# Performance work log

Measured on AMD Instinct MI355X. Metric: run time of the kernel, lower is better.

The kernel has to match this reference:

```python
import jax, jax.numpy as jnp
import numpy as np

B, S, HID = 4, 2048, 576
NH, NKV, HD = 9, 3, 64
MAXPOS, THETA = 8192, 100000.0


def rotate_half(x):
    x1, x2 = x[..., : x.shape[-1] // 2], x[..., x.shape[-1] // 2 :]
    return jnp.concatenate((-x2, x1), axis=-1)


def setup_inputs() -> dict:
    key = jax.random.key(0)
    ks = jax.random.split(key, 6)
    x = jax.random.normal(ks[0], (B, S, HID), dtype=jnp.float32)
    # RoPE tables (HuggingFace layout: freqs duplicated across halves)
    inv_freq = 1.0 / (THETA ** (np.arange(0, HD, 2, dtype=np.float32) / HD))
    freqs = np.outer(np.arange(MAXPOS, dtype=np.float32), inv_freq)
    emb = np.concatenate([freqs, freqs], axis=-1)
    cos = jnp.asarray(np.cos(emb))
    sin = jnp.asarray(np.sin(emb))
    position_ids = jnp.broadcast_to(jnp.arange(S, dtype=jnp.int64), (B, S))
    # additive causal mask [B,1,S,S]
    causal = jnp.where(
        jnp.tril(jnp.ones((S, S), dtype=bool)), 0.0, -1e9
    ).astype(jnp.float32)
    attention_mask = jnp.broadcast_to(causal, (B, 1, S, S))
    scale = 0.02
    wq = jax.random.normal(ks[1], (NH * HD, HID), dtype=jnp.float32) * scale
    wk = jax.random.normal(ks[2], (NKV * HD, HID), dtype=jnp.float32) * scale
    wv = jax.random.normal(ks[3], (NKV * HD, HID), dtype=jnp.float32) * scale
    wo = jax.random.normal(ks[4], (HID, NH * HD), dtype=jnp.float32) * scale
    return {
        "x": x, "cos": cos, "sin": sin, "position_ids": position_ids,
        "attention_mask": attention_mask,
        "wq": wq, "wk": wk, "wv": wv, "wo": wo,
    }


def reference(x, cos, sin, position_ids, attention_mask, wq, wk, wv, wo):
    b, s, _ = x.shape
    # projections (nn.Linear: y = x @ W.T), split into heads -> [B,H,S,D]
    q = (x @ wq.T).reshape(b, s, NH, HD).transpose(0, 2, 1, 3)
    k = (x @ wk.T).reshape(b, s, NKV, HD).transpose(0, 2, 1, 3)
    v = (x @ wv.T).reshape(b, s, NKV, HD).transpose(0, 2, 1, 3)
    # RoPE: cos/sin gathered per position -> [B,1,S,D], broadcast over heads
    c = cos[position_ids][:, None, :, :]
    si = sin[position_ids][:, None, :, :]
    q = q * c + rotate_half(q) * si
    k = k * c + rotate_half(k) * si
    # GQA expansion: repeat_interleave kv heads to match q heads
    k = jnp.repeat(k, NH // NKV, axis=1)
    v = jnp.repeat(v, NH // NKV, axis=1)
    scale = 1.0 / jnp.sqrt(jnp.asarray(HD, dtype=x.dtype))
    scores = jnp.einsum("bhqd,bhkd->bhqk", q, k) * scale + attention_mask
    attn = jax.nn.softmax(scores.astype(jnp.float32), axis=-1).astype(q.dtype)
    out = jnp.einsum("bhqk,bhkd->bhqd", attn, v)
    out = out.transpose(0, 2, 1, 3).reshape(b, s, NH * HD)
    return out @ wo.T
```

## Files before the change

### kernel.cpp

```cpp
#include <hip/hip_runtime.h>
#include <hip/hip_bf16.h>

#define B_    4
#define S_    2048
#define HID_  576
#define NH_   9
#define NKV_  3
#define HD_   64
#define GQ_   3

typedef __attribute__((ext_vector_type(8))) short bf16x8;
typedef __attribute__((ext_vector_type(4))) float f32x4;

__device__ __forceinline__ short f2bf(float f) {
    union { float f; unsigned int u; } v; v.f = f;
    unsigned int r = (v.u + 0x7fffu + ((v.u >> 16) & 1u)) >> 16;
    return (short)r;
}

__device__ __forceinline__ float exp2fast(float x) {
    return __builtin_amdgcn_exp2f(x);
}

__device__ __forceinline__ void async16(const void* g, void* l) {
    __builtin_amdgcn_global_load_lds(
        (const __attribute__((address_space(1))) unsigned int*)g,
        (__attribute__((address_space(3))) unsigned int*)l, 16, 0, 0);
}

#define NX_   (8192 * 576)
#define NWQ_  (576 * 576)
#define NWK_  (192 * 576)
#define NWV_  (192 * 576)
#define NWO_  (576 * 576)
#define NTOT_ (NX_ + NWQ_ + NWK_ + NWV_ + NWO_)

__global__ __launch_bounds__(256) void convert_kernel(
    const float* __restrict__ x,  const float* __restrict__ wq,
    const float* __restrict__ wk, const float* __restrict__ wv,
    const float* __restrict__ wo,
    short* __restrict__ xb, short* __restrict__ wqkvb, short* __restrict__ wob)
{
    int i4 = (blockIdx.x * 256 + threadIdx.x) * 4;
    const float* src; short* dst;
    if (i4 < NX_)                          { src = x  + i4;                          dst = xb    + i4; }
    else if (i4 < NX_ + NWQ_)              { src = wq + (i4 - NX_);                  dst = wqkvb + (i4 - NX_); }
    else if (i4 < NX_ + NWQ_ + NWK_)       { src = wk + (i4 - NX_ - NWQ_);           dst = wqkvb + (i4 - NX_); }
    else if (i4 < NX_ + NWQ_ + NWK_ + NWV_){ src = wv + (i4 - NX_ - NWQ_ - NWK_);    dst = wqkvb + (i4 - NX_); }
    else                                   { src = wo + (i4 - NX_ - NWQ_ - NWK_ - NWV_);
                                             dst = wob + (i4 - NX_ - NWQ_ - NWK_ - NWV_); }
    float4 v = *(const float4*)src;
    short4 o = make_short4(f2bf(v.x), f2bf(v.y), f2bf(v.z), f2bf(v.w));
    *(short4*)dst = o;
}

__global__ __launch_bounds__(256) void qkv_kernel(
    const short* __restrict__ xb,
    const short* __restrict__ wqkvb,
    const float* __restrict__ cosb,
    const float* __restrict__ sinb,
    short* __restrict__ Q,
    short* __restrict__ K,
    short* __restrict__ Vt)
{
    __shared__ __align__(16) short As[2][256 * 64];
    __shared__ __align__(16) short Bs[2][64 * 64];

    const int m0     = blockIdx.x * 256;
    const int nb_blk = blockIdx.y;
    const int tid  = threadIdx.x;
    const int w    = tid >> 6, lane = tid & 63;
    const int quad = lane >> 4, c = lane & 15;
    const int lr   = lane >> 3, lg = lane & 7;
    const int sw   = lg ^ lr;
    const int xg   = quad ^ (c & 7);

    auto stage = [&](int step, short* dstA, short* dstB) {
        const int k0 = step * 64;
        #pragma unroll
        for (int r = 0; r < 8; ++r) {
            int ch = w * 8 + r, R = ch * 8 + lr;
            async16(xb + (size_t)(m0 + R) * HID_ + k0 + sw * 8, (char*)dstA + ch * 1024);
        }
        #pragma unroll
        for (int r = 0; r < 2; ++r) {
            int ch = w * 2 + r, R = ch * 8 + lr;
            async16(wqkvb + (size_t)(nb_blk * 64 + R) * HID_ + k0 + sw * 8, (char*)dstB + ch * 1024);
        }
    };

    f32x4 acc[4][4];
    #pragma unroll
    for (int mt = 0; mt < 4; ++mt)
        #pragma unroll
        for (int nb = 0; nb < 4; ++nb) acc[mt][nb] = (f32x4){0.f, 0.f, 0.f, 0.f};

    stage(0, As[0], Bs[0]);

    int buf = 0;
    for (int kk = 0; kk < 9; ++kk) {
        __syncthreads();
        if (kk < 8) stage(kk + 1, As[buf ^ 1], Bs[buf ^ 1]);

        const short* a_s = As[buf];
        const short* b_s = Bs[buf];
        bf16x8 bfr[4][2];
        #pragma unroll
        for (int nb = 0; nb < 4; ++nb) {
            int row = nb * 16 + c;
            bfr[nb][0] = *(const bf16x8*)(b_s + row * 64 + xg * 8);
            bfr[nb][1] = *(const bf16x8*)(b_s + row * 64 + (xg ^ 4) * 8);
        }
        #pragma unroll
        for (int mt = 0; mt < 4; ++mt) {
            int row = w * 64 + mt * 16 + c;
            bf16x8 a0 = *(const bf16x8*)(a_s + row * 64 + xg * 8);
            bf16x8 a1 = *(const bf16x8*)(a_s + row * 64 + (xg ^ 4) * 8);
            #pragma unroll
            for (int nb = 0; nb < 4; ++nb) {
                acc[mt][nb] = __builtin_amdgcn_mfma_f32_16x16x32_bf16(a0, bfr[nb][0], acc[mt][nb], 0, 0, 0);
                acc[mt][nb] = __builtin_amdgcn_mfma_f32_16x16x32_bf16(a1, bfr[nb][1], acc[mt][nb], 0, 0, 0);
            }
        }
        buf ^= 1;
    }

    int type, head;
    if (nb_blk < NH_)            { type = 0; head = nb_blk; }
    else if (nb_blk < NH_ + NKV_){ type = 1; head = nb_blk - NH_; }
    else                         { type = 2; head = nb_blk - NH_ - NKV_; }
    const int b  = m0 >> 11;
    const int s0 = m0 & (S_ - 1);

    if (type < 2) {
        const float qs = (type == 0) ? 0.18033688f : 1.0f;
        #pragma unroll
        for (int mt = 0; mt < 4; ++mt)
            #pragma unroll
            for (int reg = 0; reg < 4; ++reg) {
                int s = s0 + w * 64 + mt * 16 + quad * 4 + reg;
                const float* cr = cosb + (size_t)s * HD_;
                const float* sr = sinb + (size_t)s * HD_;
                float a0 = acc[mt][0][reg], a1 = acc[mt][1][reg];
                float a2 = acc[mt][2][reg], a3 = acc[mt][3][reg];
                float o0 = (a0 * cr[c]      - a2 * sr[c])      * qs;
                float o1 = (a1 * cr[c + 16] - a3 * sr[c + 16]) * qs;
                float o2 = (a2 * cr[c + 32] + a0 * sr[c + 32]) * qs;
                float o3 = (a3 * cr[c + 48] + a1 * sr[c + 48]) * qs;
                short* dst = (type == 0)
                    ? Q + (((size_t)b * NH_  + head) * S_ + s) * HD_
                    : K + (((size_t)b * NKV_ + head) * S_ + s) * HD_;
                dst[c]      = f2bf(o0);
                dst[c + 16] = f2bf(o1);
                dst[c + 32] = f2bf(o2);
                dst[c + 48] = f2bf(o3);
            }
    } else {
        short* base = Vt + (((size_t)b * NKV_ + head) * HD_) * S_;
        #pragma unroll
        for (int mt = 0; mt < 4; ++mt) {
            int s4 = s0 + w * 64 + mt * 16 + quad * 4;
            #pragma unroll
            for (int nb = 0; nb < 4; ++nb) {
                int d = nb * 16 + c;
                short4 pk = make_short4(f2bf(acc[mt][nb][0]), f2bf(acc[mt][nb][1]),
                                        f2bf(acc[mt][nb][2]), f2bf(acc[mt][nb][3]));
                *(short4*)(base + (size_t)d * S_ + s4) = pk;
            }
        }
    }
}

#define PSTR 72

__global__ __launch_bounds__(256) void attn_kernel(
    const short* __restrict__ Q,
    const short* __restrict__ K,
    const short* __restrict__ Vt,
    short* __restrict__ AOb)
{
    __shared__ __align__(16) short Qs[64 * 64];
    __shared__ __align__(16) short Ks[2][64 * 64];
    __shared__ __align__(16) short Vs[2][64 * 64];
    __shared__ __align__(16) short Ps[64 * PSTR];

    const int hb = blockIdx.x;
    const int h  = hb >> 2, b = hb & 3;
    const int qt = 31 - blockIdx.y;
    const int kh = h / GQ_;
    const int tid  = threadIdx.x;
    const int w    = tid >> 6, lane = tid & 63;
    const int quad = lane >> 4, c = lane & 15;
    const int lr   = lane >> 3, lg = lane & 7;
    const int sw   = lg ^ lr;
    const int xg   = quad ^ (c & 7);

    const short* Qg = Q  + (((size_t)b * NH_  + h ) * S_ + qt * 64) * HD_;
    const short* Kg = K  + (((size_t)b * NKV_ + kh) * S_) * HD_;
    const short* Vg = Vt + (((size_t)b * NKV_ + kh) * HD_) * S_;

    #pragma unroll
    for (int r = 0; r < 2; ++r) {
        int ch = w * 2 + r, R = ch * 8 + lr;
        async16(Qg + (size_t)R * HD_ + sw * 8, (char*)Qs + ch * 1024);
    }
    #pragma unroll
    for (int r = 0; r < 4; ++r) {
        int it = w * 4 + r;
        if (it < 8) {
            int R = it * 8 + lr;
            async16(Kg + (size_t)R * HD_ + sw * 8, (char*)Ks[0] + it * 1024);
        } else {
            int R = (it - 8) * 8 + lr;
            async16(Vg + (size_t)R * S_ + sw * 8, (char*)Vs[0] + (it - 8) * 1024);
        }
    }

    bf16x8 ones;
    #pragma unroll
    for (int i = 0; i < 8; ++i) ones[i] = (short)0x3F80;

    f32x4 acc_o[4];
    #pragma unroll
    for (int nb = 0; nb < 4; ++nb) acc_o[nb] = (f32x4){0.f, 0.f, 0.f, 0.f};
    f32x4 acc_l = (f32x4){0.f, 0.f, 0.f, 0.f};

    bf16x8 aq0, aq1;

    auto do_tile = [&](const short* ks, const short* vs, bool MASK) {
        f32x4 sc[4];
        #pragma unroll
        for (int nb = 0; nb < 4; ++nb) {
            bf16x8 bk0 = *(const bf16x8*)(ks + (nb * 16 + c) * 64 + xg * 8);
            bf16x8 bk1 = *(const bf16x8*)(ks + (nb * 16 + c) * 64 + (xg ^ 4) * 8);
            f32x4 z = (f32x4){0.f, 0.f, 0.f, 0.f};
            z = __builtin_amdgcn_mfma_f32_16x16x32_bf16(aq0, bk0, z, 0, 0, 0);
            z = __builtin_amdgcn_mfma_f32_16x16x32_bf16(aq1, bk1, z, 0, 0, 0);
            sc[nb] = z;
        }
        #pragma unroll
        for (int r = 0; r < 4; ++r) {
            const int qrow = w * 16 + quad * 4 + r;
            #pragma unroll
            for (int nb = 0; nb < 4; ++nb) {
                float sv = sc[nb][r] - 4.0f;
                if (MASK && (nb * 16 + c > qrow)) sv = -1e30f;
                Ps[(w * 16 + quad * 4 + r) * PSTR + nb * 16 + c] = f2bf(exp2fast(sv));
            }
        }
        #pragma unroll
        for (int kc = 0; kc < 2; ++kc) {
            bf16x8 ap = *(const bf16x8*)(Ps + (w * 16 + c) * PSTR + quad * 8 + kc * 32);
            int pg = kc ? (xg ^ 4) : xg;
            #pragma unroll
            for (int nb = 0; nb < 4; ++nb) {
                bf16x8 bv = *(const bf16x8*)(vs + (nb * 16 + c) * 64 + pg * 8);
                acc_o[nb] = __builtin_amdgcn_mfma_f32_16x16x32_bf16(ap, bv, acc_o[nb], 0, 0, 0);
            }
            acc_l = __builtin_amdgcn_mfma_f32_16x16x32_bf16(ap, ones, acc_l, 0, 0, 0);
        }
    };

    __syncthreads();
    aq0 = *(const bf16x8*)(Qs + (w * 16 + c) * 64 + xg * 8);
    aq1 = *(const bf16x8*)(Qs + (w * 16 + c) * 64 + (xg ^ 4) * 8);

    int buf = 0;
    for (int kt = 0; kt < qt; ++kt) {
        int nxt = buf ^ 1;
        #pragma unroll
        for (int r = 0; r < 4; ++r) {
            int it = w * 4 + r;
            if (it < 8) {
                int R = it * 8 + lr;
                async16(Kg + (size_t)((kt + 1) * 64 + R) * HD_ + sw * 8,
                        (char*)Ks[nxt] + it * 1024);
            } else {
                int R = (it - 8) * 8 + lr;
                async16(Vg + (size_t)R * S_ + (kt + 1) * 64 + sw * 8,
                        (char*)Vs[nxt] + (it - 8) * 1024);
            }
        }
        do_tile(Ks[buf], Vs[buf], false);
        __syncthreads();
        buf ^= 1;
    }
    do_tile(Ks[buf], Vs[buf], true);

    #pragma unroll
    for (int r = 0; r < 4; ++r) {
        int s = qt * 64 + w * 16 + quad * 4 + r;
        float inv = 1.f / acc_l[r];
        short* dst = AOb + (((size_t)b * S_ + s) * NH_ + h) * HD_;
        #pragma unroll
        for (int nb = 0; nb < 4; ++nb)
            dst[nb * 16 + c] = f2bf(acc_o[nb][r] * inv);
    }
}

__global__ __launch_bounds__(256) void oproj_kernel(
    const short* __restrict__ AOb,
    const short* __restrict__ wob,
    float* __restrict__ out)
{
    __shared__ __align__(16) short As[2][256 * 64];
    __shared__ __align__(16) short Bs[2][64 * 64];

    const int m0 = blockIdx.x * 256;
    const int n0 = blockIdx.y * 64;
    const int tid  = threadIdx.x;
    const int w    = tid >> 6, lane = tid & 63;
    const int quad = lane >> 4, c = lane & 15;
    const int lr   = lane >> 3, lg = lane & 7;
    const int sw   = lg ^ lr;
    const int xg   = quad ^ (c & 7);

    auto stage = [&](int step, short* dstA, short* dstB) {
        const int k0 = step * 64;
        #pragma unroll
        for (int r = 0; r < 8; ++r) {
            int ch = w * 8 + r, R = ch * 8 + lr;
            async16(AOb + (size_t)(m0 + R) * HID_ + k0 + sw * 8, (char*)dstA + ch * 1024);
        }
        #pragma unroll
        for (int r = 0; r < 2; ++r) {
            int ch = w * 2 + r, R = ch * 8 + lr;
            async16(wob + (size_t)(n0 + R) * HID_ + k0 + sw * 8, (char*)dstB + ch * 1024);
        }
    };

    f32x4 acc[4][4];
    #pragma unroll
    for (int mt = 0; mt < 4; ++mt)
        #pragma unroll
        for (int nb = 0; nb < 4; ++nb) acc[mt][nb] = (f32x4){0.f, 0.f, 0.f, 0.f};

    stage(0, As[0], Bs[0]);

    int buf = 0;
    for (int kk = 0; kk < 9; ++kk) {
        __syncthreads();
        if (kk < 8) stage(kk + 1, As[buf ^ 1], Bs[buf ^ 1]);

        const short* a_s = As[buf];
        const short* b_s = Bs[buf];
        bf16x8 bfr[4][2];
        #pragma unroll
        for (int nb = 0; nb < 4; ++nb) {
            int row = nb * 16 + c;
            bfr[nb][0] = *(const bf16x8*)(b_s + row * 64 + xg * 8);
            bfr[nb][1] = *(const bf16x8*)(b_s + row * 64 + (xg ^ 4) * 8);
        }
        #pragma unroll
        for (int mt = 0; mt < 4; ++mt) {
            int row = w * 64 + mt * 16 + c;
            bf16x8 a0 = *(const bf16x8*)(a_s + row * 64 + xg * 8);
            bf16x8 a1 = *(const bf16x8*)(a_s + row * 64 + (xg ^ 4) * 8);
            #pragma unroll
            for (int nb = 0; nb < 4; ++nb) {
                acc[mt][nb] = __builtin_amdgcn_mfma_f32_16x16x32_bf16(a0, bfr[nb][0], acc[mt][nb], 0, 0, 0);
                acc[mt][nb] = __builtin_amdgcn_mfma_f32_16x16x32_bf16(a1, bfr[nb][1], acc[mt][nb], 0, 0, 0);
            }
        }
        buf ^= 1;
    }

    #pragma unroll
    for (int mt = 0; mt < 4; ++mt)
        #pragma unroll
        for (int reg = 0; reg < 4; ++reg) {
            int m = m0 + w * 64 + mt * 16 + quad * 4 + reg;
            float* dst = out + (size_t)m * HID_ + n0;
            #pragma unroll
            for (int nb = 0; nb < 4; ++nb)
                dst[nb * 16 + c] = acc[mt][nb][reg];
        }
}

extern "C" void kernel_launch(void* const* d_in, const int* in_sizes, int n_in,
                              void* d_out, int out_size, void* d_ws, size_t ws_size,
                              hipStream_t stream) {
    const float* x    = (const float*)d_in[0];
    const float* cosb = (const float*)d_in[1];
    const float* sinb = (const float*)d_in[2];
    const float* wq   = (const float*)d_in[5];
    const float* wk   = (const float*)d_in[6];
    const float* wv   = (const float*)d_in[7];
    const float* wo   = (const float*)d_in[8];

    short* xb    = (short*)d_ws;
    short* wqkvb = xb    + (size_t)NX_;
    short* wob   = wqkvb + (size_t)(NWQ_ + NWK_ + NWV_);
    short* Qb    = wob   + (size_t)NWO_;
    short* Kb    = Qb    + (size_t)B_ * NH_  * S_ * HD_;
    short* Vtb   = Kb    + (size_t)B_ * NKV_ * S_ * HD_;
    short* AOb   = Vtb   + (size_t)B_ * NKV_ * S_ * HD_;

    convert_kernel<<<dim3(NTOT_ / 4 / 256), dim3(256), 0, stream>>>(
        x, wq, wk, wv, wo, xb, wqkvb, wob);
    qkv_kernel<<<dim3(32, 15), dim3(256), 0, stream>>>(
        xb, wqkvb, cosb, sinb, Qb, Kb, Vtb);
    attn_kernel<<<dim3(36, 32), dim3(256), 0, stream>>>(Qb, Kb, Vtb, AOb);
    oproj_kernel<<<dim3(32, 9), dim3(256), 0, stream>>>(AOb, wob, (float*)d_out);
}
```

Baseline: 192.4 us.

## Fuse fp32-to-bf16 conversion into projection GEMM loaders, drop convert kernel

Removes the standalone conversion pass and has the QKV and output-projection kernels load fp32 x and weights directly. The values are packed to bf16 in registers and written into the same swizzled LDS layout after the MFMA loop, giving a register-staged software pipeline. This eliminates one launch and the write and reread of bf16 copies. In exchange, fp32 x is reread by every column block, global traffic per tile doubles, and register pressure rises.

After: 198.6 us. 1.03x slower.

```diff
diff --git a/kernel.cpp b/kernel.cpp
--- a/kernel.cpp
+++ b/kernel.cpp
@@ -18,6 +18,12 @@
     return (short)r;
 }
 
+__device__ __forceinline__ int pk2(float lo, float hi) {
+    union { __hip_bfloat162 h; int u; } v;
+    v.h = __float22bfloat162_rn(make_float2(lo, hi));
+    return v.u;
+}
+
 __device__ __forceinline__ float exp2fast(float x) {
     return __builtin_amdgcn_exp2f(x);
 }
@@ -28,35 +34,11 @@
         (__attribute__((address_space(3))) unsigned int*)l, 16, 0, 0);
 }
 
-#define NX_   (8192 * 576)
-#define NWQ_  (576 * 576)
-#define NWK_  (192 * 576)
-#define NWV_  (192 * 576)
-#define NWO_  (576 * 576)
-#define NTOT_ (NX_ + NWQ_ + NWK_ + NWV_ + NWO_)
-
-__global__ __launch_bounds__(256) void convert_kernel(
-    const float* __restrict__ x,  const float* __restrict__ wq,
-    const float* __restrict__ wk, const float* __restrict__ wv,
-    const float* __restrict__ wo,
-    short* __restrict__ xb, short* __restrict__ wqkvb, short* __restrict__ wob)
-{
-    int i4 = (blockIdx.x * 256 + threadIdx.x) * 4;
-    const float* src; short* dst;
-    if (i4 < NX_)                          { src = x  + i4;                          dst = xb    + i4; }
-    else if (i4 < NX_ + NWQ_)              { src = wq + (i4 - NX_);                  dst = wqkvb + (i4 - NX_); }
-    else if (i4 < NX_ + NWQ_ + NWK_)       { src = wk + (i4 - NX_ - NWQ_);           dst = wqkvb + (i4 - NX_); }
-    else if (i4 < NX_ + NWQ_ + NWK_ + NWV_){ src = wv + (i4 - NX_ - NWQ_ - NWK_);    dst = wqkvb + (i4 - NX_); }
-    else                                   { src = wo + (i4 - NX_ - NWQ_ - NWK_ - NWV_);
-                                             dst = wob + (i4 - NX_ - NWQ_ - NWK_ - NWV_); }
-    float4 v = *(const float4*)src;
-    short4 o = make_short4(f2bf(v.x), f2bf(v.y), f2bf(v.z), f2bf(v.w));
-    *(short4*)dst = o;
-}
-
 __global__ __launch_bounds__(256) void qkv_kernel(
-    const short* __restrict__ xb,
-    const short* __restrict__ wqkvb,
+    const float* __restrict__ x,
+    const float* __restrict__ wq,
+    const float* __restrict__ wk,
+    const float* __restrict__ wv,
     const float* __restrict__ cosb,
     const float* __restrict__ sinb,
     short* __restrict__ Q,
@@ -75,32 +57,62 @@
     const int sw   = lg ^ lr;
     const int xg   = quad ^ (c & 7);
 
-    auto stage = [&](int step, short* dstA, short* dstB) {
+    int type, head;
+    if (nb_blk < NH_)            { type = 0; head = nb_blk; }
+    else if (nb_blk < NH_ + NKV_){ type = 1; head = nb_blk - NH_; }
+    else                         { type = 2; head = nb_blk - NH_ - NKV_; }
+    const float* wsrc = (type == 0) ? wq + (size_t)head * 64 * HID_
+                      : (type == 1) ? wk + (size_t)head * 64 * HID_
+                                    : wv + (size_t)head * 64 * HID_;
+
+    f32x4 acc[4][4];
+    #pragma unroll
+    for (int mt = 0; mt < 4; ++mt)
+        #pragma unroll
+        for (int nb = 0; nb < 4; ++nb) acc[mt][nb] = (f32x4){0.f, 0.f, 0.f, 0.f};
+
+    float4 la[8][2], lb[2][2];
+    auto load_stage = [&](int step) {
         const int k0 = step * 64;
         #pragma unroll
         for (int r = 0; r < 8; ++r) {
             int ch = w * 8 + r, R = ch * 8 + lr;
-            async16(xb + (size_t)(m0 + R) * HID_ + k0 + sw * 8, (char*)dstA + ch * 1024);
+            const float* s = x + (size_t)(m0 + R) * HID_ + k0 + sw * 8;
+            la[r][0] = *(const float4*)s;
+            la[r][1] = *(const float4*)(s + 4);
         }
         #pragma unroll
         for (int r = 0; r < 2; ++r) {
             int ch = w * 2 + r, R = ch * 8 + lr;
-            async16(wqkvb + (size_t)(nb_blk * 64 + R) * HID_ + k0 + sw * 8, (char*)dstB + ch * 1024);
-        }
-    };
-
-    f32x4 acc[4][4];
-    #pragma unroll
-    for (int mt = 0; mt < 4; ++mt)
-        #pragma unroll
-        for (int nb = 0; nb < 4; ++nb) acc[mt][nb] = (f32x4){0.f, 0.f, 0.f, 0.f};
-
-    stage(0, As[0], Bs[0]);
+            const float* s = wsrc + (size_t)R * HID_ + k0 + sw * 8;
+            lb[r][0] = *(const float4*)s;
+            lb[r][1] = *(const float4*)(s + 4);
+        }
+    };
+    auto write_stage = [&](short* dstA, short* dstB) {
+        #pragma unroll
+        for (int r = 0; r < 8; ++r) {
+            int ch = w * 8 + r;
+            int4 p = { pk2(la[r][0].x, la[r][0].y), pk2(la[r][0].z, la[r][0].w),
+                       pk2(la[r][1].x, la[r][1].y), pk2(la[r][1].z, la[r][1].w) };
+            *(int4*)((char*)dstA + ch * 1024 + lane * 16) = p;
+        }
+        #pragma unroll
+        for (int r = 0; r < 2; ++r) {
+            int ch = w * 2 + r;
+            int4 p = { pk2(lb[r][0].x, lb[r][0].y), pk2(lb[r][0].z, lb[r][0].w),
+                       pk2(lb[r][1].x, lb[r][1].y), pk2(lb[r][1].z, lb[r][1].w) };
+            *(int4*)((char*)dstB + ch * 1024 + lane * 16) = p;
+        }
+    };
+
+    load_stage(0);
+    write_stage(As[0], Bs[0]);
 
     int buf = 0;
     for (int kk = 0; kk < 9; ++kk) {
         __syncthreads();
-        if (kk < 8) stage(kk + 1, As[buf ^ 1], Bs[buf ^ 1]);
+        if (kk < 8) load_stage(kk + 1);
 
         const short* a_s = As[buf];
         const short* b_s = Bs[buf];
@@ -122,13 +134,10 @@
                 acc[mt][nb] = __builtin_amdgcn_mfma_f32_16x16x32_bf16(a1, bfr[nb][1], acc[mt][nb], 0, 0, 0);
             }
         }
+        if (kk < 8) write_stage(As[buf ^ 1], Bs[buf ^ 1]);
         buf ^= 1;
     }
 
-    int type, head;
-    if (nb_blk < NH_)            { type = 0; head = nb_blk; }
-    else if (nb_blk < NH_ + NKV_){ type = 1; head = nb_blk - NH_; }
-    else                         { type = 2; head = nb_blk - NH_ - NKV_; }
     const int b  = m0 >> 11;
     const int s0 = m0 & (S_ - 1);
 
@@ -300,7 +309,7 @@
 
 __global__ __launch_bounds__(256) void oproj_kernel(
     const short* __restrict__ AOb,
-    const short* __restrict__ wob,
+    const float* __restrict__ wo,
     float* __restrict__ out)
 {
     __shared__ __align__(16) short As[2][256 * 64];
@@ -315,18 +324,33 @@
     const int sw   = lg ^ lr;
     const int xg   = quad ^ (c & 7);
 
-    auto stage = [&](int step, short* dstA, short* dstB) {
+    float4 lb[2][2];
+    auto loadB = [&](int step) {
+        const int k0 = step * 64;
+        #pragma unroll
+        for (int r = 0; r < 2; ++r) {
+            int ch = w * 2 + r, R = ch * 8 + lr;
+            const float* s = wo + (size_t)(n0 + R) * HID_ + k0 + sw * 8;
+            lb[r][0] = *(const float4*)s;
+            lb[r][1] = *(const float4*)(s + 4);
+        }
+    };
+    auto writeB = [&](short* dstB) {
+        #pragma unroll
+        for (int r = 0; r < 2; ++r) {
+            int ch = w * 2 + r;
+            int4 p = { pk2(lb[r][0].x, lb[r][0].y), pk2(lb[r][0].z, lb[r][0].w),
+                       pk2(lb[r][1].x, lb[r][1].y), pk2(lb[r][1].z, lb[r][1].w) };
+            *(int4*)((char*)dstB + ch * 1024 + lane * 16) = p;
+        }
+    };
+    auto stageA = [&](int step, short* dstA) {
         const int k0 = step * 64;
         #pragma unroll
         for (int r = 0; r < 8; ++r) {
             int ch = w * 8 + r, R = ch * 8 + lr;
             async16(AOb + (size_t)(m0 + R) * HID_ + k0 + sw * 8, (char*)dstA + ch * 1024);
         }
-        #pragma unroll
-        for (int r = 0; r < 2; ++r) {
-            int ch = w * 2 + r, R = ch * 8 + lr;
-            async16(wob + (size_t)(n0 + R) * HID_ + k0 + sw * 8, (char*)dstB + ch * 1024);
-        }
     };
 
     f32x4 acc[4][4];
@@ -335,12 +359,14 @@
         #pragma unroll
         for (int nb = 0; nb < 4; ++nb) acc[mt][nb] = (f32x4){0.f, 0.f, 0.f, 0.f};
 
-    stage(0, As[0], Bs[0]);
+    stageA(0, As[0]);
+    loadB(0);
+    writeB(Bs[0]);
 
     int buf = 0;
     for (int kk = 0; kk < 9; ++kk) {
         __syncthreads();
-        if (kk < 8) stage(kk + 1, As[buf ^ 1], Bs[buf ^ 1]);
+        if (kk < 8) { stageA(kk + 1, As[buf ^ 1]); loadB(kk + 1); }
 
         const short* a_s = As[buf];
         const short* b_s = Bs[buf];
@@ -362,6 +388,7 @@
                 acc[mt][nb] = __builtin_amdgcn_mfma_f32_16x16x32_bf16(a1, bfr[nb][1], acc[mt][nb], 0, 0, 0);
             }
         }
+        if (kk < 8) writeB(Bs[buf ^ 1]);
         buf ^= 1;
     }
 
@@ -388,18 +415,13 @@
     const float* wv   = (const float*)d_in[7];
     const float* wo   = (const float*)d_in[8];
 
-    short* xb    = (short*)d_ws;
-    short* wqkvb = xb    + (size_t)NX_;
-    short* wob   = wqkvb + (size_t)(NWQ_ + NWK_ + NWV_);
-    short* Qb    = wob   + (size_t)NWO_;
-    short* Kb    = Qb    + (size_t)B_ * NH_  * S_ * HD_;
-    short* Vtb   = Kb    + (size_t)B_ * NKV_ * S_ * HD_;
-    short* AOb   = Vtb   + (size_t)B_ * NKV_ * S_ * HD_;
-
-    convert_kernel<<<dim3(NTOT_ / 4 / 256), dim3(256), 0, stream>>>(
-        x, wq, wk, wv, wo, xb, wqkvb, wob);
+    short* Qb  = (short*)d_ws;
+    short* Kb  = Qb  + (size_t)B_ * NH_  * S_ * HD_;
+    short* Vtb = Kb  + (size_t)B_ * NKV_ * S_ * HD_;
+    short* AOb = Vtb + (size_t)B_ * NKV_ * S_ * HD_;
+
     qkv_kernel<<<dim3(32, 15), dim3(256), 0, stream>>>(
-        xb, wqkvb, cosb, sinb, Qb, Kb, Vtb);
+        x, wq, wk, wv, cosb, sinb, Qb, Kb, Vtb);
     attn_kernel<<<dim3(36, 32), dim3(256), 0, stream>>>(Qb, Kb, Vtb, AOb);
-    oproj_kernel<<<dim3(32, 9), dim3(256), 0, stream>>>(AOb, wob, (float*)d_out);
-}
+    oproj_kernel<<<dim3(32, 9), dim3(256), 0, stream>>>(AOb, wo, (float*)d_out);
+}
```
